# Performance work log

Hardware: AMD Instinct MI355X
Metric: run time of the kernel (lower is better)

The kernel has to match this reference:

```python
import jax, jax.numpy as jnp
import numpy as np

BN_EPS = 1e-5  # PyTorch BatchNorm1d default eps (Dice's self.eps is unused by its bn)

def _bn(x):
    # training-mode BatchNorm1d without affine: batch mean / biased variance
    m = jnp.mean(x, axis=0)
    v = jnp.var(x, axis=0)
    return (x - m) * jax.lax.rsqrt(v + BN_EPS)

def _dice(x, alpha):
    p = jax.nn.sigmoid(_bn(x))
    return alpha * (1.0 - p) * x + p * x

def setup_inputs():
    key = jax.random.key(0)
    ks = jax.random.split(key, 48)
    B, L = 8192, 200
    Vu, Vd, Va, Vs, Vg, Vt, Vf = 100001, 1001, 50001, 20001, 20001, 501, 100001
    f = jnp.float32
    s = 0.05
    inp = {}
    inp['dense'] = jax.random.normal(ks[0], (B, 16), f)
    inp['userid'] = jax.random.randint(ks[1], (B,), 0, Vu)
    inp['device'] = jax.random.randint(ks[2], (B,), 0, Vd)
    inp['authorid'] = jax.random.randint(ks[3], (B,), 0, Va)
    inp['bgm_song_id'] = jax.random.randint(ks[4], (B,), 0, Vs)
    inp['bgm_singer_id'] = jax.random.randint(ks[5], (B,), 0, Vg)
    inp['manual_tag'] = jax.random.randint(ks[6], (B,), 0, Vt)
    inp['feedid'] = jax.random.randint(ks[7], (B,), 0, Vf)
    inp['seq_ids'] = jax.random.randint(ks[8], (B, L), 0, Vf)
    inp['seq_len'] = jax.random.randint(ks[9], (B,), 1, L + 1)
    # embedding tables (dims hard-coded in the torch module)
    inp['emb_userid'] = s * jax.random.normal(ks[10], (Vu, 16), f)
    inp['emb_device'] = s * jax.random.normal(ks[11], (Vd, 2), f)
    inp['emb_authorid'] = s * jax.random.normal(ks[12], (Va, 4), f)
    inp['emb_song'] = s * jax.random.normal(ks[13], (Vs, 4), f)
    inp['emb_singer'] = s * jax.random.normal(ks[14], (Vg, 4), f)
    inp['emb_tag'] = s * jax.random.normal(ks[15], (Vt, 4), f)
    inp['emb_feedid'] = s * jax.random.normal(ks[16], (Vf, 16), f)
    inp['emb_seq'] = s * jax.random.normal(ks[17], (Vf, 16), f)
    # attention MLP: 4*16 -> 64 -> 32 -> 1
    inp['aW1'] = s * jax.random.normal(ks[18], (64, 64), f)
    inp['ab1'] = jnp.zeros((64,), f)
    inp['aW2'] = s * jax.random.normal(ks[19], (64, 32), f)
    inp['ab2'] = jnp.zeros((32,), f)
    inp['aW3'] = s * jax.random.normal(ks[20], (32, 1), f)
    inp['ab3'] = jnp.zeros((1,), f)
    # FCN stack: 82 -> 512 -> 256 -> 128 -> 1, Dice alpha + affine BN per layer
    dims = [82, 512, 256, 128]
    for i in range(3):
        inp[f'W{i}'] = s * jax.random.normal(ks[21 + i], (dims[i], dims[i + 1]), f)
        inp[f'b{i}'] = jnp.zeros((dims[i + 1],), f)
        inp[f'alpha{i}'] = jnp.zeros((dims[i + 1],), f)
        inp[f'g{i}'] = jnp.ones((dims[i + 1],), f)
        inp[f'beta{i}'] = jnp.zeros((dims[i + 1],), f)
    inp['Wout'] = s * jax.random.normal(ks[30], (128, 1), f)
    inp['bout'] = jnp.zeros((1,), f)
    return inp

def _forward(dense, userid, device, authorid, bgm_song_id, bgm_singer_id, manual_tag,
             feedid, seq_ids, seq_len,
             emb_userid, emb_device, emb_authorid, emb_song, emb_singer, emb_tag,
             emb_feedid, emb_seq,
             aW1, ab1, aW2, ab2, aW3, ab3,
             W0, b0, alpha0, g0, beta0,
             W1, b1, alpha1, g1, beta1,
             W2, b2, alpha2, g2, beta2,
             Wout, bout):
    B, L = seq_ids.shape
    # embedding lookups
    cat_embs = [emb_userid[userid], emb_device[device], emb_authorid[authorid],
                emb_song[bgm_song_id], emb_singer[bgm_singer_id], emb_tag[manual_tag]]
    q = emb_feedid[feedid]            # [B, 16]
    keys = emb_seq[seq_ids]           # [B, L, 16]
    # DIN attention: cross features + 3-layer MLP score
    qe = jnp.broadcast_to(q[:, None, :], keys.shape)
    cross = jnp.concatenate([qe, keys, qe - keys, qe * keys], axis=2)  # [B, L, 64]
    h = jax.nn.relu(cross @ aW1 + ab1)
    h = jax.nn.relu(h @ aW2 + ab2)
    score = (h @ aW3 + ab3)[..., 0]   # [B, L]
    mask = jnp.arange(L)[None, :] < seq_len[:, None]
    w = jnp.where(mask, score, 0.0)   # is_softmax=False branch
    att_out = jnp.sum(w[:, :, None] * keys, axis=1)  # [B, 16]
    # dense MLP stack with Dice + affine BN (dropout is identity at eval)
    net = jnp.concatenate([dense] + cat_embs + [q, att_out], axis=1)  # [B, 82]
    for W, b, a, g, be in ((W0, b0, alpha0, g0, beta0),
                           (W1, b1, alpha1, g1, beta1),
                           (W2, b2, alpha2, g2, beta2)):
        net = net @ W + b
        net = _dice(net, a)
        net = g * _bn(net) + be
    logit = net @ Wout + bout
    prob = jax.nn.sigmoid(logit)
    emb_vars = jnp.concatenate(cat_embs + [q, att_out], axis=1)
    l2_reg = 0.2 * jnp.mean(jnp.linalg.norm(emb_vars, axis=1))
    return prob, logit, l2_reg

def reference(dense, userid, device, authorid, bgm_song_id, bgm_singer_id, manual_tag,
              feedid, seq_ids, seq_len,
              emb_userid, emb_device, emb_authorid, emb_song, emb_singer, emb_tag,
              emb_feedid, emb_seq,
              aW1, ab1, aW2, ab2, aW3, ab3,
              W0, b0, alpha0, g0, beta0,
              W1, b1, alpha1, g1, beta1,
              W2, b2, alpha2, g2, beta2,
              Wout, bout):
    return _forward(dense, userid, device, authorid, bgm_song_id, bgm_singer_id, manual_tag,
                    feedid, seq_ids, seq_len,
                    emb_userid, emb_device, emb_authorid, emb_song, emb_singer, emb_tag,
                    emb_feedid, emb_seq,
                    aW1, ab1, aW2, ab2, aW3, ab3,
                    W0, b0, alpha0, g0, beta0,
                    W1, b1, alpha1, g1, beta1,
                    W2, b2, alpha2, g2, beta2,
                    Wout, bout)
```

## Files before the change

### kernel.cpp

```cpp
#include <hip/hip_runtime.h>
#include <hip/hip_bf16.h>

#define B_ 8192
#define L_ 200

typedef __attribute__((ext_vector_type(4))) short s4v;
typedef __attribute__((ext_vector_type(8))) short s8v;
typedef __attribute__((ext_vector_type(16))) float f32x16;

__device__ __forceinline__ short f2bf(float f) {
    union { float f; unsigned u; } v; v.f = f;
    unsigned r = (v.u + 0x7fffu + ((v.u >> 16) & 1u)) >> 16;
    return (short)r;
}
__device__ __forceinline__ float bf2f(short s) {
    union { unsigned u; float f; } v; v.u = ((unsigned)(unsigned short)s) << 16;
    return v.f;
}
__device__ __forceinline__ unsigned cvtpk(float a, float b) {
    unsigned r;
    asm("v_cvt_pk_bf16_f32 %0, %1, %2" : "=v"(r) : "v"(a), "v"(b));
    return r;
}

#define OFF_ATT   0
#define OFF_NETBF (OFF_ATT + B_*16)
#define OFF_X     (OFF_NETBF + B_*64)
#define OFF_D0    (OFF_X + B_*512)
#define OFF_D1    (OFF_D0 + B_*256)
#define OFF_D2    (OFF_D1 + B_*128)
#define OFF_ACC   (OFF_D2 + B_*64)
#define OFF_NORM  (OFF_ACC + 12*512)
#define OFF_PREP  (OFF_NORM + 1)
#define OFF_W0T   (OFF_PREP + 4096)
#define OFF_W1T   (OFF_W0T + 32768)
#define OFF_W2T   (OFF_W1T + 65536)
#define OFF_FB1   (OFF_W2T + 16384)
#define OFF_FB2   (OFF_FB1 + 256)

__global__ __launch_bounds__(256) void prep_w(
    const float* __restrict__ aW1, const float* __restrict__ aW2,
    const float* __restrict__ W0, float* __restrict__ wsP, short* __restrict__ W0T,
    float* __restrict__ acc, float* __restrict__ fb)
{
    const int t = threadIdx.x;
    if (blockIdx.x == 0) {
        short* W1BC = (short*)wsP;
        short* W1D  = (short*)(wsP + 512);
        float* W1AC = wsP + 1024;
        short* W2F  = (short*)(wsP + 2048);
        for (int idx = t; idx < 1024; idx += 256) {
            int r = idx & 7, l = (idx >> 3) & 63, mt = idx >> 9;
            int i = ((l >> 5) << 3) + r, j = mt * 32 + (l & 31);
            W1BC[idx] = f2bf(aW1[(16 + i) * 64 + j] - aW1[(32 + i) * 64 + j]);
            W1D[idx]  = f2bf(aW1[(48 + i) * 64 + j]);
        }
        for (int idx = t; idx < 1024; idx += 256) {
            int i = idx & 15, j = idx >> 4;
            W1AC[idx] = aW1[i * 64 + j] + aW1[(32 + i) * 64 + j];
        }
        for (int idx = t; idx < 2048; idx += 256) {
            int r = idx & 7, l = (idx >> 3) & 63, ks = idx >> 9;
            int j2 = ks * 16 + ((l >> 5) << 3) + r, n2 = l & 31;
            W2F[idx] = f2bf(aW2[j2 * 32 + n2]);
        }
    } else if (blockIdx.x == 33) {
        for (int i = t; i < 12 * 512 + 1; i += 256) acc[i] = 0.f;
        if (t < 256 + 128) fb[t] = 0.f;
    } else {
        for (int idx = (blockIdx.x - 1) * 256 + t; idx < 512 * 128; idx += 32 * 256) {
            int n = idx & 511, k = idx >> 9;
            W0T[n * 128 + k] = (k < 82) ? f2bf(W0[k * 512 + n]) : (short)0;
        }
    }
}

__global__ __launch_bounds__(256) void prep_fold(
    const float* __restrict__ W, const float* __restrict__ bias,
    const float* __restrict__ sD, const float* __restrict__ qD,
    const float* __restrict__ g, const float* __restrict__ be,
    float invB, int K, int N,
    short* __restrict__ WT, float* __restrict__ fb)
{
    __shared__ short tile[64][65];
    __shared__ float sclS[64], sftS[64];
    __shared__ float red[256];
    const int t = threadIdx.x;
    const int bn = blockIdx.x * 64, bk = blockIdx.y * 64;

    if (t < 64) {
        const int k = bk + t;
        float m = sD[k] * invB;
        float v = fmaf(-m, m, qD[k] * invB);
        float sc = g[k] * rsqrtf(v + 1e-5f);
        sclS[t] = sc;
        sftS[t] = be[k] - m * sc;
    }
    __syncthreads();

    const int nn = t & 63, kk0 = (t >> 6) * 16;
    float part = 0.f;
    #pragma unroll
    for (int i = 0; i < 16; ++i) {
        const int kk = kk0 + i;
        float w = W[(size_t)(bk + kk) * N + bn + nn];
        tile[kk][nn] = f2bf(sclS[kk] * w);
        part = fmaf(sftS[kk], w, part);
    }
    red[t] = part;
    __syncthreads();

    {
        const int n = t >> 2, kp = (t & 3) * 16;
        short* dst = &WT[(size_t)(bn + n) * K + bk + kp];
        #pragma unroll
        for (int i = 0; i < 16; ++i) dst[i] = tile[kp + i][n];
    }
    if (t < 64) {
        float s = red[t] + red[t + 64] + red[t + 128] + red[t + 192];
        if (blockIdx.y == 0) s += bias[bn + t];
        atomicAdd(&fb[bn + t], s);
    }
}

__global__ __launch_bounds__(256) void attn_k(
    const int* __restrict__ feedid, const int* __restrict__ seq_ids,
    const int* __restrict__ seq_len,
    const float* __restrict__ e_feed, const float* __restrict__ e_seq,
    const float* __restrict__ ab1, const float* __restrict__ ab2,
    const float* __restrict__ ab3, const float* __restrict__ aW3,
    const float* __restrict__ wsP, float* __restrict__ att)
{
    __shared__ short KL[224 * 20];
    __shared__ short KQ[224 * 20];
    __shared__ int   sidS[224];
    __shared__ float qS[16];
    __shared__ float qtS[64];
    __shared__ float w3S[32], ab2S[32];
    __shared__ float wS[224];
    __shared__ float pS[16 * 16];

    const short* W1BC = (const short*)wsP;
    const short* W1D  = (const short*)(wsP + 512);
    const float* W1AC = wsP + 1024;
    const short* W2F  = (const short*)(wsP + 2048);

    const int b = blockIdx.x, t = threadIdx.x;

    if (t < 16) qS[t] = e_feed[(size_t)feedid[b] * 16 + t];
    if (t >= 32 && t < 64) w3S[t - 32] = aW3[t - 32];
    if (t >= 64 && t < 96) ab2S[t - 64] = ab2[t - 64];
    if (t < 200) sidS[t] = seq_ids[(size_t)b * L_ + t];
    __syncthreads();

    for (int idx = t; idx < 800; idx += 256) {
        int row = idx >> 2, p = idx & 3, c0 = p * 4;
        int sid = sidS[row];
        const float4 f4 = ((const float4*)(e_seq + (size_t)sid * 16))[p];
        uint2 kk, kq;
        kk.x = cvtpk(f4.x, f4.y);
        kk.y = cvtpk(f4.z, f4.w);
        kq.x = cvtpk(f4.x * qS[c0],     f4.y * qS[c0 + 1]);
        kq.y = cvtpk(f4.z * qS[c0 + 2], f4.w * qS[c0 + 3]);
        *(uint2*)&KL[row * 20 + c0] = kk;
        *(uint2*)&KQ[row * 20 + c0] = kq;
    }
    if (t < 96) {
        int row = 200 + (t >> 2), c0 = (t & 3) * 4;
        uint2 z = {0u, 0u};
        *(uint2*)&KL[row * 20 + c0] = z;
        *(uint2*)&KQ[row * 20 + c0] = z;
    }
    if (t < 64) {
        float s = ab1[t];
        #pragma unroll
        for (int i = 0; i < 16; ++i) s = fmaf(qS[i], W1AC[t * 16 + i], s);
        qtS[t] = s;
    }

    const int h = (t >> 5) & 1, l31 = t & 31, l63 = t & 63, wv = t >> 6;

    s8v w1bcF[2], w1dF[2], w2f[4];
    #pragma unroll
    for (int mt = 0; mt < 2; ++mt) {
        w1bcF[mt] = *(const s8v*)&W1BC[(mt * 64 + l63) * 8];
        w1dF[mt]  = *(const s8v*)&W1D[(mt * 64 + l63) * 8];
    }
    #pragma unroll
    for (int ks = 0; ks < 4; ++ks)
        w2f[ks] = *(const s8v*)&W2F[(ks * 64 + l63) * 8];

    __syncthreads();

    union U8 { s8v s; unsigned u[4]; };
    const float ab3v = ab3[0];
    const int len = seq_len[b];

    for (int m = wv; m < 7; m += 4) {
        const int row = m * 32 + l31;
        s8v bK, bKQ;
        {
            s4v lo = *(const s4v*)&KL[row * 20 + h * 8];
            s4v hi = *(const s4v*)&KL[row * 20 + h * 8 + 4];
            bK[0] = lo[0]; bK[1] = lo[1]; bK[2] = lo[2]; bK[3] = lo[3];
            bK[4] = hi[0]; bK[5] = hi[1]; bK[6] = hi[2]; bK[7] = hi[3];
            s4v lo2 = *(const s4v*)&KQ[row * 20 + h * 8];
            s4v hi2 = *(const s4v*)&KQ[row * 20 + h * 8 + 4];
            bKQ[0] = lo2[0]; bKQ[1] = lo2[1]; bKQ[2] = lo2[2]; bKQ[3] = lo2[3];
            bKQ[4] = hi2[0]; bKQ[5] = hi2[1]; bKQ[6] = hi2[2]; bKQ[7] = hi2[3];
        }

        f32x16 c2;
        #pragma unroll
        for (int i = 0; i < 16; ++i) c2[i] = 0.f;

        #pragma unroll
        for (int mt = 0; mt < 2; ++mt) {
            f32x16 c;
            #pragma unroll
            for (int i = 0; i < 16; ++i) c[i] = 0.f;
            c = __builtin_amdgcn_mfma_f32_32x32x16_bf16(w1bcF[mt], bK,  c, 0, 0, 0);
            c = __builtin_amdgcn_mfma_f32_32x32x16_bf16(w1dF[mt],  bKQ, c, 0, 0, 0);

            unsigned pk[8], pks[8];
            #pragma unroll
            for (int i = 0; i < 8; ++i) {
                int r0 = 2 * i, r1 = r0 + 1;
                float v0 = fmaxf(c[r0] + qtS[mt * 32 + (r0 & 3) + 8 * (r0 >> 2) + 4 * h], 0.f);
                float v1 = fmaxf(c[r1] + qtS[mt * 32 + (r1 & 3) + 8 * (r1 >> 2) + 4 * h], 0.f);
                pk[i] = cvtpk(v0, v1);
                pks[i] = __shfl_xor(pk[i], 32);
            }
            {
                U8 bf2;
                bf2.u[0] = h ? pks[2] : pk[0];
                bf2.u[1] = h ? pks[3] : pk[1];
                bf2.u[2] = h ? pk[2]  : pks[0];
                bf2.u[3] = h ? pk[3]  : pks[1];
                c2 = __builtin_amdgcn_mfma_f32_32x32x16_bf16(w2f[mt * 2], bf2.s, c2, 0, 0, 0);
            }
            {
                U8 bf2;
                bf2.u[0] = h ? pks[6] : pk[4];
                bf2.u[1] = h ? pks[7] : pk[5];
                bf2.u[2] = h ? pk[6]  : pks[4];
                bf2.u[3] = h ? pk[7]  : pks[5];
                c2 = __builtin_amdgcn_mfma_f32_32x32x16_bf16(w2f[mt * 2 + 1], bf2.s, c2, 0, 0, 0);
            }
        }

        float part = 0.f;
        #pragma unroll
        for (int r = 0; r < 16; ++r) {
            int n2 = (r & 3) + 8 * (r >> 2) + 4 * h;
            part = fmaf(fmaxf(c2[r] + ab2S[n2], 0.f), w3S[n2], part);
        }
        float tot = part + __shfl_xor(part, 32) + ab3v;
        if (h == 0) wS[row] = (row < len) ? tot : 0.f;
    }
    __syncthreads();

    {
        const int c = t & 15, ch = t >> 4, r0 = ch * 14;
        float s = 0.f;
        #pragma unroll
        for (int i = 0; i < 14; ++i)
            s = fmaf(wS[r0 + i], bf2f(KL[(r0 + i) * 20 + c]), s);
        pS[ch * 16 + c] = s;
    }
    __syncthreads();
    if (t < 16) {
        float s = 0.f;
        #pragma unroll
        for (int ch = 0; ch < 16; ++ch) s += pS[ch * 16 + t];
        att[(size_t)b * 16 + t] = s;
    }
}

__global__ __launch_bounds__(256) void build_net(
    const float* __restrict__ dense,
    const int* __restrict__ userid, const int* __restrict__ device_,
    const int* __restrict__ authorid, const int* __restrict__ song,
    const int* __restrict__ singer, const int* __restrict__ tag,
    const int* __restrict__ feedid,
    const float* __restrict__ e_user, const float* __restrict__ e_dev,
    const float* __restrict__ e_auth, const float* __restrict__ e_song,
    const float* __restrict__ e_singer, const float* __restrict__ e_tag,
    const float* __restrict__ e_feed,
    const float* __restrict__ att, short* __restrict__ nbf,
    float* __restrict__ norm_acc)
{
    const int b = blockIdx.x * 256 + threadIdx.x;
    float row[82];
    const float* d = dense + (size_t)b * 16;
    #pragma unroll
    for (int i = 0; i < 16; ++i) row[i] = d[i];
    const float* eu = e_user + (size_t)userid[b] * 16;
    #pragma unroll
    for (int i = 0; i < 16; ++i) row[16 + i] = eu[i];
    const float* ed = e_dev + (size_t)device_[b] * 2;
    row[32] = ed[0]; row[33] = ed[1];
    const float* ea = e_auth + (size_t)authorid[b] * 4;
    #pragma unroll
    for (int i = 0; i < 4; ++i) row[34 + i] = ea[i];
    const float* es = e_song + (size_t)song[b] * 4;
    #pragma unroll
    for (int i = 0; i < 4; ++i) row[38 + i] = es[i];
    const float* eg = e_singer + (size_t)singer[b] * 4;
    #pragma unroll
    for (int i = 0; i < 4; ++i) row[42 + i] = eg[i];
    const float* et = e_tag + (size_t)tag[b] * 4;
    #pragma unroll
    for (int i = 0; i < 4; ++i) row[46 + i] = et[i];
    const float* ef = e_feed + (size_t)feedid[b] * 16;
    #pragma unroll
    for (int i = 0; i < 16; ++i) row[50 + i] = ef[i];
    const float* at = att + (size_t)b * 16;
    #pragma unroll
    for (int i = 0; i < 16; ++i) row[66 + i] = at[i];

    float sq = 0.f;
    #pragma unroll
    for (int i = 16; i < 82; ++i) sq = fmaf(row[i], row[i], sq);

    union { unsigned w[64]; uint4 w4[16]; } U;
    #pragma unroll
    for (int i = 0; i < 41; ++i) U.w[i] = cvtpk(row[2 * i], row[2 * i + 1]);
    #pragma unroll
    for (int i = 41; i < 64; ++i) U.w[i] = 0u;
    uint4* op = (uint4*)(nbf + (size_t)b * 128);
    #pragma unroll
    for (int c = 0; c < 16; ++c) op[c] = U.w4[c];

    float nrm = sqrtf(sq);
    nrm += __shfl_xor(nrm, 32); nrm += __shfl_xor(nrm, 16);
    nrm += __shfl_xor(nrm, 8);  nrm += __shfl_xor(nrm, 4);
    nrm += __shfl_xor(nrm, 2);  nrm += __shfl_xor(nrm, 1);
    if ((threadIdx.x & 63) == 0) atomicAdd(norm_acc, nrm);
}

__global__ __launch_bounds__(256) void gemm_mfma_stats(
    const short* __restrict__ A, int lda,
    const short* __restrict__ BT, int ldb,
    const float* __restrict__ bias,
    float* __restrict__ C, int N, int K,
    float* __restrict__ sout, float* __restrict__ qout)
{
    __shared__ short As[64 * 68];
    __shared__ short Bs[64 * 68];
    __shared__ float colS[64], colQ[64];

    const int bm = blockIdx.y * 64, bn = blockIdx.x * 64;
    const int t = threadIdx.x;
    const int wv = t >> 6, l31 = t & 31, h = (t >> 5) & 1;
    const int qr = wv >> 1, qc = wv & 1;

    if (t < 64) { colS[t] = 0.f; colQ[t] = 0.f; }

    const int row0 = t >> 3, part = (t & 7) * 8;
    s8v ar[2], br[2];
    #pragma unroll
    for (int i = 0; i < 2; ++i) {
        ar[i] = *(const s8v*)&A[(size_t)(bm + row0 + i * 32) * lda + part];
        br[i] = *(const s8v*)&BT[(size_t)(bn + row0 + i * 32) * ldb + part];
    }

    f32x16 acc;
    #pragma unroll
    for (int i = 0; i < 16; ++i) acc[i] = 0.f;

    const int nk = K >> 6;
    for (int kc = 0; kc < nk; ++kc) {
        #pragma unroll
        for (int i = 0; i < 2; ++i) {
            *(s8v*)&As[(row0 + i * 32) * 68 + part] = ar[i];
            *(s8v*)&Bs[(row0 + i * 32) * 68 + part] = br[i];
        }
        __syncthreads();
        if (kc + 1 < nk) {
            const int k0 = (kc + 1) << 6;
            #pragma unroll
            for (int i = 0; i < 2; ++i) {
                ar[i] = *(const s8v*)&A[(size_t)(bm + row0 + i * 32) * lda + k0 + part];
                br[i] = *(const s8v*)&BT[(size_t)(bn + row0 + i * 32) * ldb + k0 + part];
            }
        }
        #pragma unroll
        for (int ks = 0; ks < 4; ++ks) {
            const s8v af = *(const s8v*)&As[(qr * 32 + l31) * 68 + ks * 16 + h * 8];
            const s8v bf = *(const s8v*)&Bs[(qc * 32 + l31) * 68 + ks * 16 + h * 8];
            acc = __builtin_amdgcn_mfma_f32_32x32x16_bf16(af, bf, acc, 0, 0, 0);
        }
        __syncthreads();
    }

    const int col = bn + qc * 32 + l31;
    const float bv = bias[col];
    float s = 0.f, q = 0.f;
    #pragma unroll
    for (int r = 0; r < 16; ++r) {
        const int row = bm + qr * 32 + (r & 3) + 8 * (r >> 2) + 4 * h;
        float x = acc[r] + bv;
        C[(size_t)row * N + col] = x;
        s += x; q = fmaf(x, x, q);
    }
    s += __shfl_xor(s, 32);
    q += __shfl_xor(q, 32);
    if (h == 0) {
        atomicAdd(&colS[qc * 32 + l31], s);
        atomicAdd(&colQ[qc * 32 + l31], q);
    }
    __syncthreads();
    if (t < 64) {
        atomicAdd(&sout[bn + t], colS[t]);
        atomicAdd(&qout[bn + t], colQ[t]);
    }
}

__global__ __launch_bounds__(256) void dice_stats(
    const float* __restrict__ X, short* __restrict__ D,
    const float* __restrict__ sin_, const float* __restrict__ qin_,
    const float* __restrict__ alpha,
    float* __restrict__ sout, float* __restrict__ qout,
    int N, float invB)
{
    __shared__ float cS[64], cQ[64];
    const int t = threadIdx.x;
    const int col = blockIdx.x * 64 + (t & 63);
    const int r0 = blockIdx.y * 64 + (t >> 6);
    if (t < 64) { cS[t] = 0.f; cQ[t] = 0.f; }
    __syncthreads();

    const float m = sin_[col] * invB;
    const float v = fmaf(-m, m, qin_[col] * invB);
    const float rs = rsqrtf(v + 1e-5f);
    const float al = alpha[col];

    float s = 0.f, q = 0.f;
    #pragma unroll
    for (int i = 0; i < 16; ++i) {
        const int r = r0 + i * 4;
        const float x = X[(size_t)r * N + col];
        const float xn = (x - m) * rs;
        const float p = 1.f / (1.f + __expf(-xn));
        const float d = x * (p + al * (1.f - p));
        D[(size_t)r * N + col] = f2bf(d);
        s += d; q = fmaf(d, d, q);
    }
    atomicAdd(&cS[t & 63], s);
    atomicAdd(&cQ[t & 63], q);
    __syncthreads();
    if (t < 64) {
        atomicAdd(&sout[blockIdx.x * 64 + t], cS[t]);
        atomicAdd(&qout[blockIdx.x * 64 + t], cQ[t]);
    }
}

__global__ __launch_bounds__(256) void final_k(
    const short* __restrict__ Y, const float* __restrict__ Wout,
    const float* __restrict__ bout, const float* __restrict__ norm_acc,
    const float* __restrict__ sD, const float* __restrict__ qD,
    const float* __restrict__ g, const float* __restrict__ be,
    float invB, float* __restrict__ out)
{
    const int wv = threadIdx.x >> 6, lane = threadIdx.x & 63;
    const int b = blockIdx.x * 4 + wv;
    const short* y = Y + (size_t)b * 128;

    float s = 0.f;
    #pragma unroll
    for (int hh = 0; hh < 2; ++hh) {
        const int c = hh * 64 + lane;
        const float m = sD[c] * invB;
        const float v = fmaf(-m, m, qD[c] * invB);
        const float yn = g[c] * (bf2f(y[c]) - m) * rsqrtf(v + 1e-5f) + be[c];
        s = fmaf(yn, Wout[c], s);
    }
    s += __shfl_xor(s, 32); s += __shfl_xor(s, 16);
    s += __shfl_xor(s, 8);  s += __shfl_xor(s, 4);
    s += __shfl_xor(s, 2);  s += __shfl_xor(s, 1);
    if (lane == 0) {
        float logit = s + bout[0];
        out[B_ + b] = logit;
        out[b] = 1.f / (1.f + __expf(-logit));
    }
    if (blockIdx.x == 0 && threadIdx.x == 0)
        out[2 * B_] = 0.2f * norm_acc[0] / (float)B_;
}

extern "C" void kernel_launch(void* const* d_in, const int* in_sizes, int n_in,
                              void* d_out, int out_size, void* d_ws, size_t ws_size,
                              hipStream_t stream)
{
    const float* dense    = (const float*)d_in[0];
    const int*   userid   = (const int*)d_in[1];
    const int*   device_  = (const int*)d_in[2];
    const int*   authorid = (const int*)d_in[3];
    const int*   song     = (const int*)d_in[4];
    const int*   singer   = (const int*)d_in[5];
    const int*   tag      = (const int*)d_in[6];
    const int*   feedid   = (const int*)d_in[7];
    const int*   seq_ids  = (const int*)d_in[8];
    const int*   seq_len  = (const int*)d_in[9];
    const float* e_user   = (const float*)d_in[10];
    const float* e_dev    = (const float*)d_in[11];
    const float* e_auth   = (const float*)d_in[12];
    const float* e_song   = (const float*)d_in[13];
    const float* e_singer = (const float*)d_in[14];
    const float* e_tag    = (const float*)d_in[15];
    const float* e_feed   = (const float*)d_in[16];
    const float* e_seq    = (const float*)d_in[17];
    const float* aW1 = (const float*)d_in[18];
    const float* ab1 = (const float*)d_in[19];
    const float* aW2 = (const float*)d_in[20];
    const float* ab2 = (const float*)d_in[21];
    const float* aW3 = (const float*)d_in[22];
    const float* ab3 = (const float*)d_in[23];
    const float* W0 = (const float*)d_in[24]; const float* b0 = (const float*)d_in[25];
    const float* al0 = (const float*)d_in[26]; const float* g0 = (const float*)d_in[27];
    const float* be0 = (const float*)d_in[28];
    const float* W1 = (const float*)d_in[29]; const float* b1 = (const float*)d_in[30];
    const float* al1 = (const float*)d_in[31]; const float* g1 = (const float*)d_in[32];
    const float* be1 = (const float*)d_in[33];
    const float* W2 = (const float*)d_in[34]; const float* b2 = (const float*)d_in[35];
    const float* al2 = (const float*)d_in[36]; const float* g2 = (const float*)d_in[37];
    const float* be2 = (const float*)d_in[38];
    const float* Wout = (const float*)d_in[39]; const float* bout = (const float*)d_in[40];

    float* ws    = (float*)d_ws;
    float* att   = ws + OFF_ATT;
    short* netbf = (short*)(ws + OFF_NETBF);
    float* X     = ws + OFF_X;
    short* d0    = (short*)(ws + OFF_D0);
    short* d1    = (short*)(ws + OFF_D1);
    short* d2    = (short*)(ws + OFF_D2);
    float* acc   = ws + OFF_ACC;
    float* norm  = ws + OFF_NORM;
    float* prep  = ws + OFF_PREP;
    short* W0T   = (short*)(ws + OFF_W0T);
    short* W1T   = (short*)(ws + OFF_W1T);
    short* W2T   = (short*)(ws + OFF_W2T);
    float* fb1   = ws + OFF_FB1;
    float* fb2   = ws + OFF_FB2;
    float* out   = (float*)d_out;

    float* sX0 = acc + 0*512;  float* qX0 = acc + 1*512;
    float* sD0 = acc + 2*512;  float* qD0 = acc + 3*512;
    float* sX1 = acc + 4*512;  float* qX1 = acc + 5*512;
    float* sD1 = acc + 6*512;  float* qD1 = acc + 7*512;
    float* sX2 = acc + 8*512;  float* qX2 = acc + 9*512;
    float* sD2 = acc + 10*512; float* qD2 = acc + 11*512;

    const float invB = 1.f / (float)B_;

    hipLaunchKernelGGL(prep_w, dim3(34), dim3(256), 0, stream,
                       aW1, aW2, W0, prep, W0T, acc, fb1);

    hipLaunchKernelGGL(attn_k, dim3(B_), dim3(256), 0, stream,
                       feedid, seq_ids, seq_len, e_feed, e_seq,
                       ab1, ab2, ab3, aW3, prep, att);

    hipLaunchKernelGGL(build_net, dim3(B_/256), dim3(256), 0, stream,
                       dense, userid, device_, authorid, song, singer, tag, feedid,
                       e_user, e_dev, e_auth, e_song, e_singer, e_tag, e_feed,
                       att, netbf, norm);

    hipLaunchKernelGGL(gemm_mfma_stats, dim3(512/64, B_/64), dim3(256), 0, stream,
                       netbf, 128, W0T, 128, b0, X, 512, 128, sX0, qX0);
    hipLaunchKernelGGL(dice_stats, dim3(512/64, B_/64), dim3(256), 0, stream,
                       X, d0, sX0, qX0, al0, sD0, qD0, 512, invB);
    hipLaunchKernelGGL(prep_fold, dim3(256/64, 512/64), dim3(256), 0, stream,
                       W1, b1, sD0, qD0, g0, be0, invB, 512, 256, W1T, fb1);

    hipLaunchKernelGGL(gemm_mfma_stats, dim3(256/64, B_/64), dim3(256), 0, stream,
                       d0, 512, W1T, 512, fb1, X, 256, 512, sX1, qX1);
    hipLaunchKernelGGL(dice_stats, dim3(256/64, B_/64), dim3(256), 0, stream,
                       X, d1, sX1, qX1, al1, sD1, qD1, 256, invB);
    hipLaunchKernelGGL(prep_fold, dim3(128/64, 256/64), dim3(256), 0, stream,
                       W2, b2, sD1, qD1, g1, be1, invB, 256, 128, W2T, fb2);

    hipLaunchKernelGGL(gemm_mfma_stats, dim3(128/64, B_/64), dim3(256), 0, stream,
                       d1, 256, W2T, 256, fb2, X, 128, 256, sX2, qX2);
    hipLaunchKernelGGL(dice_stats, dim3(128/64, B_/64), dim3(256), 0, stream,
                       X, d2, sX2, qX2, al2, sD2, qD2, 128, invB);

    hipLaunchKernelGGL(final_k, dim3(B_/4), dim3(256), 0, stream,
                       d2, Wout, bout, norm, sD2, qD2, g2, be2, invB, out);
}
```

Before: 275.9 us.

## Fuse net-row build into attention kernel and store pre-activation GEMM outputs as bf16

Merges the build_net kernel into attn_k: each block gathers its row's dense and categorical embeddings into shared memory, appends the attention output, packs the 82-wide row to bf16 and accumulates the L2 norm with one atomic per block. This drops a kernel launch and the round trip of the attention output through global memory. Separately, the GEMM outputs X are now written as bf16 instead of fp32, halving traffic into dice_stats at some precision cost, since Dice normalisation is computed from the rounded values while the stats still use fp32. Per-lane bias and weight constants in the attention MLP are also hoisted from shared memory into registers.

```diff
diff --git a/kernel.cpp b/kernel.cpp
--- a/kernel.cpp
+++ b/kernel.cpp
@@ -23,8 +23,7 @@
     return r;
 }
 
-#define OFF_ATT   0
-#define OFF_NETBF (OFF_ATT + B_*16)
+#define OFF_NETBF 0
 #define OFF_X     (OFF_NETBF + B_*64)
 #define OFF_D0    (OFF_X + B_*512)
 #define OFF_D1    (OFF_D0 + B_*256)
@@ -129,7 +128,15 @@
     const float* __restrict__ e_feed, const float* __restrict__ e_seq,
     const float* __restrict__ ab1, const float* __restrict__ ab2,
     const float* __restrict__ ab3, const float* __restrict__ aW3,
-    const float* __restrict__ wsP, float* __restrict__ att)
+    const float* __restrict__ wsP,
+    const float* __restrict__ dense,
+    const int* __restrict__ userid, const int* __restrict__ device_,
+    const int* __restrict__ authorid, const int* __restrict__ song,
+    const int* __restrict__ singer, const int* __restrict__ tag,
+    const float* __restrict__ e_user, const float* __restrict__ e_dev,
+    const float* __restrict__ e_auth, const float* __restrict__ e_song,
+    const float* __restrict__ e_singer, const float* __restrict__ e_tag,
+    short* __restrict__ nbf, float* __restrict__ norm_acc)
 {
     __shared__ short KL[224 * 20];
     __shared__ short KQ[224 * 20];
@@ -139,6 +146,7 @@
     __shared__ float w3S[32], ab2S[32];
     __shared__ float wS[224];
     __shared__ float pS[16 * 16];
+    __shared__ float nrS[88];
 
     const short* W1BC = (const short*)wsP;
     const short* W1D  = (const short*)(wsP + 512);
@@ -147,9 +155,16 @@
 
     const int b = blockIdx.x, t = threadIdx.x;
 
-    if (t < 16) qS[t] = e_feed[(size_t)feedid[b] * 16 + t];
+    if (t < 16) { float q = e_feed[(size_t)feedid[b] * 16 + t]; qS[t] = q; nrS[50 + t] = q; }
     if (t >= 32 && t < 64) w3S[t - 32] = aW3[t - 32];
     if (t >= 64 && t < 96) ab2S[t - 64] = ab2[t - 64];
+    if (t >= 96 && t < 112) nrS[t - 96] = dense[(size_t)b * 16 + (t - 96)];
+    if (t >= 112 && t < 128) nrS[16 + (t - 112)] = e_user[(size_t)userid[b] * 16 + (t - 112)];
+    if (t >= 128 && t < 130) nrS[32 + (t - 128)] = e_dev[(size_t)device_[b] * 2 + (t - 128)];
+    if (t >= 130 && t < 134) nrS[34 + (t - 130)] = e_auth[(size_t)authorid[b] * 4 + (t - 130)];
+    if (t >= 134 && t < 138) nrS[38 + (t - 134)] = e_song[(size_t)song[b] * 4 + (t - 134)];
+    if (t >= 138 && t < 142) nrS[42 + (t - 138)] = e_singer[(size_t)singer[b] * 4 + (t - 138)];
+    if (t >= 142 && t < 146) nrS[46 + (t - 142)] = e_tag[(size_t)tag[b] * 4 + (t - 142)];
     if (t < 200) sidS[t] = seq_ids[(size_t)b * L_ + t];
     __syncthreads();
 
@@ -191,6 +206,16 @@
         w2f[ks] = *(const s8v*)&W2F[(ks * 64 + l63) * 8];
 
     __syncthreads();
+
+    float qtR0[16], qtR1[16], ab2R[16], w3R[16];
+    #pragma unroll
+    for (int r = 0; r < 16; ++r) {
+        const int cr = (r & 3) + 8 * (r >> 2) + 4 * h;
+        qtR0[r] = qtS[cr];
+        qtR1[r] = qtS[32 + cr];
+        ab2R[r] = ab2S[cr];
+        w3R[r]  = w3S[cr];
+    }
 
     union U8 { s8v s; unsigned u[4]; };
     const float ab3v = ab3[0];
@@ -226,8 +251,10 @@
             #pragma unroll
             for (int i = 0; i < 8; ++i) {
                 int r0 = 2 * i, r1 = r0 + 1;
-                float v0 = fmaxf(c[r0] + qtS[mt * 32 + (r0 & 3) + 8 * (r0 >> 2) + 4 * h], 0.f);
-                float v1 = fmaxf(c[r1] + qtS[mt * 32 + (r1 & 3) + 8 * (r1 >> 2) + 4 * h], 0.f);
+                float q0 = mt ? qtR1[r0] : qtR0[r0];
+                float q1 = mt ? qtR1[r1] : qtR0[r1];
+                float v0 = fmaxf(c[r0] + q0, 0.f);
+                float v1 = fmaxf(c[r1] + q1, 0.f);
                 pk[i] = cvtpk(v0, v1);
                 pks[i] = __shfl_xor(pk[i], 32);
             }
@@ -251,10 +278,8 @@
 
         float part = 0.f;
         #pragma unroll
-        for (int r = 0; r < 16; ++r) {
-            int n2 = (r & 3) + 8 * (r >> 2) + 4 * h;
-            part = fmaf(fmaxf(c2[r] + ab2S[n2], 0.f), w3S[n2], part);
-        }
+        for (int r = 0; r < 16; ++r)
+            part = fmaf(fmaxf(c2[r] + ab2R[r], 0.f), w3R[r], part);
         float tot = part + __shfl_xor(part, 32) + ab3v;
         if (h == 0) wS[row] = (row < len) ? tot : 0.f;
     }
@@ -273,77 +298,30 @@
         float s = 0.f;
         #pragma unroll
         for (int ch = 0; ch < 16; ++ch) s += pS[ch * 16 + t];
-        att[(size_t)b * 16 + t] = s;
-    }
-}
-
-__global__ __launch_bounds__(256) void build_net(
-    const float* __restrict__ dense,
-    const int* __restrict__ userid, const int* __restrict__ device_,
-    const int* __restrict__ authorid, const int* __restrict__ song,
-    const int* __restrict__ singer, const int* __restrict__ tag,
-    const int* __restrict__ feedid,
-    const float* __restrict__ e_user, const float* __restrict__ e_dev,
-    const float* __restrict__ e_auth, const float* __restrict__ e_song,
-    const float* __restrict__ e_singer, const float* __restrict__ e_tag,
-    const float* __restrict__ e_feed,
-    const float* __restrict__ att, short* __restrict__ nbf,
-    float* __restrict__ norm_acc)
-{
-    const int b = blockIdx.x * 256 + threadIdx.x;
-    float row[82];
-    const float* d = dense + (size_t)b * 16;
-    #pragma unroll
-    for (int i = 0; i < 16; ++i) row[i] = d[i];
-    const float* eu = e_user + (size_t)userid[b] * 16;
-    #pragma unroll
-    for (int i = 0; i < 16; ++i) row[16 + i] = eu[i];
-    const float* ed = e_dev + (size_t)device_[b] * 2;
-    row[32] = ed[0]; row[33] = ed[1];
-    const float* ea = e_auth + (size_t)authorid[b] * 4;
-    #pragma unroll
-    for (int i = 0; i < 4; ++i) row[34 + i] = ea[i];
-    const float* es = e_song + (size_t)song[b] * 4;
-    #pragma unroll
-    for (int i = 0; i < 4; ++i) row[38 + i] = es[i];
-    const float* eg = e_singer + (size_t)singer[b] * 4;
-    #pragma unroll
-    for (int i = 0; i < 4; ++i) row[42 + i] = eg[i];
-    const float* et = e_tag + (size_t)tag[b] * 4;
-    #pragma unroll
-    for (int i = 0; i < 4; ++i) row[46 + i] = et[i];
-    const float* ef = e_feed + (size_t)feedid[b] * 16;
-    #pragma unroll
-    for (int i = 0; i < 16; ++i) row[50 + i] = ef[i];
-    const float* at = att + (size_t)b * 16;
-    #pragma unroll
-    for (int i = 0; i < 16; ++i) row[66 + i] = at[i];
-
-    float sq = 0.f;
-    #pragma unroll
-    for (int i = 16; i < 82; ++i) sq = fmaf(row[i], row[i], sq);
-
-    union { unsigned w[64]; uint4 w4[16]; } U;
-    #pragma unroll
-    for (int i = 0; i < 41; ++i) U.w[i] = cvtpk(row[2 * i], row[2 * i + 1]);
-    #pragma unroll
-    for (int i = 41; i < 64; ++i) U.w[i] = 0u;
-    uint4* op = (uint4*)(nbf + (size_t)b * 128);
-    #pragma unroll
-    for (int c = 0; c < 16; ++c) op[c] = U.w4[c];
-
-    float nrm = sqrtf(sq);
-    nrm += __shfl_xor(nrm, 32); nrm += __shfl_xor(nrm, 16);
-    nrm += __shfl_xor(nrm, 8);  nrm += __shfl_xor(nrm, 4);
-    nrm += __shfl_xor(nrm, 2);  nrm += __shfl_xor(nrm, 1);
-    if ((threadIdx.x & 63) == 0) atomicAdd(norm_acc, nrm);
+        nrS[66 + t] = s;
+    }
+    __syncthreads();
+
+    if (t < 64) {
+        unsigned w = 0u;
+        float sq = 0.f;
+        if (t < 41) {
+            float a = nrS[2 * t], c = nrS[2 * t + 1];
+            w = cvtpk(a, c);
+            if (t >= 8) sq = fmaf(a, a, c * c);
+        }
+        ((unsigned*)nbf)[(size_t)b * 64 + t] = w;
+        sq += __shfl_xor(sq, 32); sq += __shfl_xor(sq, 16); sq += __shfl_xor(sq, 8);
+        sq += __shfl_xor(sq, 4);  sq += __shfl_xor(sq, 2);  sq += __shfl_xor(sq, 1);
+        if (t == 0) atomicAdd(norm_acc, sqrtf(sq));
+    }
 }
 
 __global__ __launch_bounds__(256) void gemm_mfma_stats(
     const short* __restrict__ A, int lda,
     const short* __restrict__ BT, int ldb,
     const float* __restrict__ bias,
-    float* __restrict__ C, int N, int K,
+    short* __restrict__ C, int N, int K,
     float* __restrict__ sout, float* __restrict__ qout)
 {
     __shared__ short As[64 * 68];
@@ -401,7 +379,7 @@
     for (int r = 0; r < 16; ++r) {
         const int row = bm + qr * 32 + (r & 3) + 8 * (r >> 2) + 4 * h;
         float x = acc[r] + bv;
-        C[(size_t)row * N + col] = x;
+        C[(size_t)row * N + col] = f2bf(x);
         s += x; q = fmaf(x, x, q);
     }
     s += __shfl_xor(s, 32);
@@ -418,7 +396,7 @@
 }
 
 __global__ __launch_bounds__(256) void dice_stats(
-    const float* __restrict__ X, short* __restrict__ D,
+    const short* __restrict__ X, short* __restrict__ D,
     const float* __restrict__ sin_, const float* __restrict__ qin_,
     const float* __restrict__ alpha,
     float* __restrict__ sout, float* __restrict__ qout,
@@ -440,7 +418,7 @@
     #pragma unroll
     for (int i = 0; i < 16; ++i) {
         const int r = r0 + i * 4;
-        const float x = X[(size_t)r * N + col];
+        const float x = bf2f(X[(size_t)r * N + col]);
         const float xn = (x - m) * rs;
         const float p = 1.f / (1.f + __expf(-xn));
         const float d = x * (p + al * (1.f - p));
@@ -528,9 +506,8 @@
     const float* Wout = (const float*)d_in[39]; const float* bout = (const float*)d_in[40];
 
     float* ws    = (float*)d_ws;
-    float* att   = ws + OFF_ATT;
     short* netbf = (short*)(ws + OFF_NETBF);
-    float* X     = ws + OFF_X;
+    short* Xbf   = (short*)(ws + OFF_X);
     short* d0    = (short*)(ws + OFF_D0);
     short* d1    = (short*)(ws + OFF_D1);
     short* d2    = (short*)(ws + OFF_D2);
@@ -558,31 +535,29 @@
 
     hipLaunchKernelGGL(attn_k, dim3(B_), dim3(256), 0, stream,
                        feedid, seq_ids, seq_len, e_feed, e_seq,
-                       ab1, ab2, ab3, aW3, prep, att);
-
-    hipLaunchKernelGGL(build_net, dim3(B_/256), dim3(256), 0, stream,
-                       dense, userid, device_, authorid, song, singer, tag, feedid,
-                       e_user, e_dev, e_auth, e_song, e_singer, e_tag, e_feed,
-                       att, netbf, norm);
+                       ab1, ab2, ab3, aW3, prep,
+                       dense, userid, device_, authorid, song, singer, tag,
+                       e_user, e_dev, e_auth, e_song, e_singer, e_tag,
+                       netbf, norm);
 
     hipLaunchKernelGGL(gemm_mfma_stats, dim3(512/64, B_/64), dim3(256), 0, stream,
-                       netbf, 128, W0T, 128, b0, X, 512, 128, sX0, qX0);
+                       netbf, 128, W0T, 128, b0, Xbf, 512, 128, sX0, qX0);
     hipLaunchKernelGGL(dice_stats, dim3(512/64, B_/64), dim3(256), 0, stream,
-                       X, d0, sX0, qX0, al0, sD0, qD0, 512, invB);
+                       Xbf, d0, sX0, qX0, al0, sD0, qD0, 512, invB);
     hipLaunchKernelGGL(prep_fold, dim3(256/64, 512/64), dim3(256), 0, stream,
                        W1, b1, sD0, qD0, g0, be0, invB, 512, 256, W1T, fb1);
 
     hipLaunchKernelGGL(gemm_mfma_stats, dim3(256/64, B_/64), dim3(256), 0, stream,
-                       d0, 512, W1T, 512, fb1, X, 256, 512, sX1, qX1);
+                       d0, 512, W1T, 512, fb1, Xbf, 256, 512, sX1, qX1);
     hipLaunchKernelGGL(dice_stats, dim3(256/64, B_/64), dim3(256), 0, stream,
-                       X, d1, sX1, qX1, al1, sD1, qD1, 256, invB);
+                       Xbf, d1, sX1, qX1, al1, sD1, qD1, 256, invB);
     hipLaunchKernelGGL(prep_fold, dim3(128/64, 256/64), dim3(256), 0, stream,
                        W2, b2, sD1, qD1, g1, be1, invB, 256, 128, W2T, fb2);
 
     hipLaunchKernelGGL(gemm_mfma_stats, dim3(128/64, B_/64), dim3(256), 0, stream,
-                       d1, 256, W2T, 256, fb2, X, 128, 256, sX2, qX2);
+                       d1, 256, W2T, 256, fb2, Xbf, 128, 256, sX2, qX2);
     hipLaunchKernelGGL(dice_stats, dim3(128/64, B_/64), dim3(256), 0, stream,
-                       X, d2, sX2, qX2, al2, sD2, qD2, 128, invB);
+                       Xbf, d2, sX2, qX2, al2, sD2, qD2, 128, invB);
 
     hipLaunchKernelGGL(final_k, dim3(B_/4), dim3(256), 0, stream,
                        d2, Wout, bout, norm, sD2, qD2, g2, be2, invB, out);
```

Result: slower. 497.1 us (+80.2%).
